# Optimization experiments

Hardware: AMD Instinct MI355X
Metric: run time of the kernel (lower is better)

The kernel has to match this reference:

```python
import jax, jax.numpy as jnp
import numpy as np

N = 100000
C = 128
VEC = 16
GRID = 128
TEMP = 1.0
REP = C // VEC


def _offsets_cube():
    r = [-1, 0, 1]
    return np.array([[i, j, k] for i in r for j in r for k in r], dtype=np.int64)


def _offsets_cross(d):
    offs = [[0, 0, 0]]
    for ax in range(3):
        for s in (-d, d):
            o = [0, 0, 0]
            o[ax] = s
            offs.append(o)
    return np.array(offs, dtype=np.int64)


def _build_nbr(coords, lut, offs):
    # coords [N,3] int, lut: flat grid -> voxel idx or -1. Returns [K,N] int32, -1 = missing.
    maps = []
    for o in offs:
        nc = coords + o
        valid = np.all((nc >= 0) & (nc < GRID), axis=1)
        flat = nc[:, 0] * GRID * GRID + nc[:, 1] * GRID + nc[:, 2]
        idx = np.where(valid, lut[np.clip(flat, 0, GRID ** 3 - 1)], -1)
        maps.append(idx)
    return jnp.asarray(np.stack(maps).astype(np.int32))


def setup_inputs() -> dict:
    rng = np.random.default_rng(0)
    flat = rng.choice(GRID ** 3, size=N, replace=False)
    coords = np.stack([flat // (GRID * GRID), (flat // GRID) % GRID, flat % GRID], axis=1)
    lut = np.full(GRID ** 3, -1, dtype=np.int64)
    lut[flat] = np.arange(N)
    nbr_cross2 = _build_nbr(coords, lut, _offsets_cross(2))  # expert 0: HYPER_CROSS dil=2, K=7
    nbr_cube = _build_nbr(coords, lut, _offsets_cube())       # expert 1: HYPER_CUBE dil=1, K=27
    nbr_cross3 = _build_nbr(coords, lut, _offsets_cross(3))  # expert 2: HYPER_CROSS dil=3, K=7

    ks = jax.random.split(jax.random.key(0), 10)
    s = lambda k, shape, sc: jax.random.normal(k, shape, jnp.float32) * sc
    return dict(
        x=s(ks[0], (N, C), 1.0),
        v1_w=s(ks[1], (27, C, C), 0.05),
        v1_g=jnp.ones((C,), jnp.float32), v1_b=jnp.zeros((C,), jnp.float32),
        v2_w=s(ks[2], (C, C), 0.05),
        v2_g=jnp.ones((C,), jnp.float32), v2_b=jnp.zeros((C,), jnp.float32),
        q_w=s(ks[3], (C, VEC), 0.05),
        q_g=jnp.ones((VEC,), jnp.float32), q_b=jnp.zeros((VEC,), jnp.float32),
        cb0=s(ks[4], (7, C), 0.1),
        cb1=s(ks[5], (27, C), 0.1),
        cb2=s(ks[6], (7, C), 0.1),
        out_w=s(ks[7], (C, C), 0.05),
        out_g=jnp.ones((C,), jnp.float32), out_b=jnp.zeros((C,), jnp.float32),
        nbr_cross2=nbr_cross2, nbr_cube=nbr_cube, nbr_cross3=nbr_cross3,
    )


def _bn(x, g, b, eps=1e-5):
    m = x.mean(0)
    v = x.var(0)
    return (x - m) * jax.lax.rsqrt(v + eps) * g + b


def _sparse_conv(x, nbr, W):
    # full sparse conv: out[i] = sum_k W[k] @ x[nbr[k,i]] over valid neighbors
    out = jnp.zeros((x.shape[0], W.shape[2]), x.dtype)
    for k in range(W.shape[0]):  # fixed small K, structural loop
        idx = nbr[k]
        g = jnp.where((idx >= 0)[:, None], x[jnp.clip(idx, 0)], 0.0)
        out = out + g @ W[k]
    return out


def _chanwise_conv(x, nbr, kern):
    # MinkowskiChannelwiseConvolution: out[i,c] = sum_k kern[k,c] * x[nbr[k,i],c]
    out = jnp.zeros_like(x)
    for k in range(kern.shape[0]):
        idx = nbr[k]
        out = out + jnp.where((idx >= 0)[:, None], x[jnp.clip(idx, 0)], 0.0) * kern[k]
    return out


def _pairwise_score(q, nbr):
    # pairwise qk: mean over valid neighbors j of q_i * q_j (per channel) -> [N, VEC]
    acc = jnp.zeros_like(q)
    cnt = jnp.zeros((q.shape[0], 1), q.dtype)
    for k in range(nbr.shape[0]):
        idx = nbr[k]
        valid = (idx >= 0)[:, None]
        acc = acc + jnp.where(valid, q[jnp.clip(idx, 0)], 0.0)
        cnt = cnt + valid.astype(q.dtype)
    return q * acc / jnp.maximum(cnt, 1.0)


def reference(x, v1_w, v1_g, v1_b, v2_w, v2_g, v2_b, q_w, q_g, q_b,
              cb0, cb1, cb2, out_w, out_g, out_b,
              nbr_cross2, nbr_cube, nbr_cross3):
    # value branch: 3x3 ConvBNReLU -> 1x1 ConvBNReLU
    v = jax.nn.relu(_bn(_sparse_conv(x, nbr_cube, v1_w), v1_g, v1_b))
    v = jax.nn.relu(_bn(v @ v2_w, v2_g, v2_b))
    # query: 1x1 ConvBNReLU -> [N, VEC]
    q = jax.nn.relu(_bn(x @ q_w, q_g, q_b))
    # M=3 channelwise codebook expert convs on the value features
    cb_outs = [
        _chanwise_conv(v, nbr_cross2, cb0),
        _chanwise_conv(v, nbr_cube, cb1),
        _chanwise_conv(v, nbr_cross3, cb2),
    ]
    # pairwise attention scores per expert neighborhood -> [N, VEC, M]
    scores = jnp.stack([
        _pairwise_score(q, nbr_cross2),
        _pairwise_score(q, nbr_cube),
        _pairwise_score(q, nbr_cross3),
    ], axis=-1)
    attn = jax.nn.softmax(scores / TEMP, axis=-1)
    attn = jnp.repeat(attn, REP, axis=1)  # expand_vec_dim: [N, C, M]
    out = sum(attn[:, :, m] * cb_outs[m] for m in range(3))
    out = jax.nn.relu(_bn(out @ out_w, out_g, out_b))
    return out + x  # residual (inplanes == planes, downsample is identity)
```

## Files before the change

### kernel.cpp

```cpp
#include <hip/hip_runtime.h>

#define NN 100000
#define C 128
#define VEC 16
#define AROW 136
#define GCAP 240000

typedef __bf16 bfx8 __attribute__((ext_vector_type(8)));
typedef float f32x4 __attribute__((ext_vector_type(4)));

__device__ inline unsigned pack_bf2(float a, float b) {
    unsigned ua = __float_as_uint(a);
    unsigned ub = __float_as_uint(b);
    ua = (ua + 0x7fffu + ((ua >> 16) & 1u)) >> 16;
    ub = (ub + 0x7fffu + ((ub >> 16) & 1u)) >> 16;
    return ua | (ub << 16);
}
__device__ inline unsigned short bf1(float a) {
    unsigned u = __float_as_uint(a);
    return (unsigned short)((u + 0x7fffu + ((u >> 16) & 1u)) >> 16);
}

__device__ inline void wconv_body(const float* __restrict__ W, unsigned short* __restrict__ Wf, int F) {
    int e = F & 7, l = (F >> 3) & 63, nt = (F >> 9) & 7, ks = (F >> 12) & 3, kt = F >> 14;
    int cin = ks * 32 + (l >> 4) * 8 + e;
    int cout = nt * 16 + (l & 15);
    Wf[F] = bf1(W[((size_t)kt * C + cin) * C + cout]);
}

__global__ __launch_bounds__(256) void prep(const float* __restrict__ v1w, const float* __restrict__ v2w,
                                            const float* __restrict__ outw, const float* __restrict__ x,
                                            unsigned short* __restrict__ v1f, unsigned short* __restrict__ v2f,
                                            unsigned short* __restrict__ outf, unsigned short* __restrict__ xh) {
    int b = blockIdx.x, tid = threadIdx.x;
    if (b < 1728)       wconv_body(v1w, v1f, b * 256 + tid);
    else if (b < 1792)  wconv_body(v2w, v2f, (b - 1728) * 256 + tid);
    else if (b < 1856)  wconv_body(outw, outf, (b - 1792) * 256 + tid);
    else {
        const int total8 = NN * C / 8;
        for (int t = (b - 1856) * 256 + tid; t < total8; t += 1024 * 256) {
            float4 xa = *reinterpret_cast<const float4*>(x + (size_t)t * 8);
            float4 xb = *reinterpret_cast<const float4*>(x + (size_t)t * 8 + 4);
            uint4 pk;
            pk.x = pack_bf2(xa.x, xa.y); pk.y = pack_bf2(xa.z, xa.w);
            pk.z = pack_bf2(xb.x, xb.y); pk.w = pack_bf2(xb.z, xb.w);
            *reinterpret_cast<uint4*>(&xh[(size_t)t * 8]) = pk;
        }
    }
}

__global__ __launch_bounds__(256) void compactA(const int* __restrict__ nbr, int* __restrict__ cnt,
                                                int* __restrict__ slotmap, int* __restrict__ pairs,
                                                unsigned* __restrict__ maskbuf) {
    const int k = blockIdx.x / 49, cb = blockIdx.x % 49, tid = threadIdx.x;
    const int i0 = cb * 2048 + tid * 8;
    int j[8]; int lc = 0;
#pragma unroll
    for (int t = 0; t < 8; ++t) {
        int i = i0 + t;
        j[t] = (i < NN) ? nbr[(size_t)k * NN + i] : -1;
        lc += (j[t] >= 0);
    }
    __shared__ int ls[256]; __shared__ int sbase;
    ls[tid] = lc; __syncthreads();
    for (int off = 1; off < 256; off <<= 1) {
        int v = (tid >= off) ? ls[tid - off] : 0;
        __syncthreads();
        ls[tid] += v;
        __syncthreads();
    }
    if (tid == 255) sbase = atomicAdd(&cnt[k], ls[255]);
    __syncthreads();
    int slot = sbase + ls[tid] - lc;
    for (int t = 0; t < 8; ++t) {
        int i = i0 + t; if (i >= NN) break;
        int s = -1;
        if (j[t] >= 0) {
            s = slot++;
            pairs[(size_t)k * NN + s] = j[t];
            atomicOr(&maskbuf[i], 1u << k);
        }
        slotmap[(size_t)k * NN + i] = s;
    }
}

__global__ void prefixA2(int* __restrict__ hdr) {
    if (threadIdx.x == 0) {
        int co = 0, go = 0;
        for (int k = 0; k < 27; ++k) {
            hdr[32 + k] = co; hdr[64 + k] = go;
            int nch = (hdr[k] + 31) / 32;
            co += nch; go += nch * 32;
        }
        hdr[32 + 27] = co;
    }
}

__global__ __launch_bounds__(256) void convB(const unsigned short* __restrict__ xh, const int* __restrict__ pairs,
                                             const int* __restrict__ hdr, const bfx8* __restrict__ Wf,
                                             unsigned short* __restrict__ g) {
    const int tid = threadIdx.x, l = tid & 63, w = tid >> 6, rr = tid >> 4, gg = tid & 15;
    __shared__ int sco[28], scnt[27], sgo[27];
    __shared__ unsigned short Ash[32 * AROW];
    __shared__ unsigned short Osh[32 * AROW];
    if (tid < 28) sco[tid] = hdr[32 + tid];
    if (tid < 27) { scnt[tid] = hdr[tid]; sgo[tid] = hdr[64 + tid]; }
    __syncthreads();
    const int tot = sco[27];
    for (int t = blockIdx.x; t < tot; t += gridDim.x) {
        int lo = 0, hi = 26;
        while (lo < hi) { int mid = (lo + hi + 1) >> 1; if (sco[mid] <= t) lo = mid; else hi = mid - 1; }
        const int k = lo, c = t - sco[k], cntk = scnt[k];
        const int srow = c * 32;
        const size_t gbase = (size_t)(sgo[k] + srow) * C;
#pragma unroll
        for (int h = 0; h < 2; ++h) {
            int row = srow + h * 16 + rr;
            uint4 pk = {0u, 0u, 0u, 0u};
            if (row < cntk) {
                int j = pairs[(size_t)k * NN + row];
                pk = *reinterpret_cast<const uint4*>(xh + (size_t)j * C + gg * 8);
            }
            *reinterpret_cast<uint4*>(&Ash[(h * 16 + rr) * AROW + gg * 8]) = pk;
        }
        __syncthreads();
        f32x4 a00 = {0.f,0.f,0.f,0.f}, a01 = {0.f,0.f,0.f,0.f};
        f32x4 a10 = {0.f,0.f,0.f,0.f}, a11 = {0.f,0.f,0.f,0.f};
        const unsigned short* ar0 = &Ash[(l & 15) * AROW + (l >> 4) * 8];
        const unsigned short* ar1 = &Ash[(16 + (l & 15)) * AROW + (l >> 4) * 8];
#pragma unroll
        for (int ks = 0; ks < 4; ++ks) {
            bfx8 b0 = Wf[((k * 4 + ks) * 8 + 2 * w) * 64 + l];
            bfx8 b1 = Wf[((k * 4 + ks) * 8 + 2 * w + 1) * 64 + l];
            bfx8 f0 = *reinterpret_cast<const bfx8*>(ar0 + ks * 32);
            bfx8 f1 = *reinterpret_cast<const bfx8*>(ar1 + ks * 32);
            a00 = __builtin_amdgcn_mfma_f32_16x16x32_bf16(f0, b0, a00, 0, 0, 0);
            a01 = __builtin_amdgcn_mfma_f32_16x16x32_bf16(f0, b1, a01, 0, 0, 0);
            a10 = __builtin_amdgcn_mfma_f32_16x16x32_bf16(f1, b0, a10, 0, 0, 0);
            a11 = __builtin_amdgcn_mfma_f32_16x16x32_bf16(f1, b1, a11, 0, 0, 0);
        }
#pragma unroll
        for (int r = 0; r < 4; ++r) {
            int row = (l >> 4) * 4 + r;
            Osh[row * AROW + w * 32 + (l & 15)]        = bf1(a00[r]);
            Osh[row * AROW + w * 32 + 16 + (l & 15)]   = bf1(a01[r]);
            Osh[(16 + row) * AROW + w * 32 + (l & 15)] = bf1(a10[r]);
            Osh[(16 + row) * AROW + w * 32 + 16 + (l & 15)] = bf1(a11[r]);
        }
        __syncthreads();
#pragma unroll
        for (int h = 0; h < 2; ++h) {
            int row = h * 16 + rr;
            uint4 v = *reinterpret_cast<uint4*>(&Osh[row * AROW + gg * 8]);
            *reinterpret_cast<uint4*>(&g[gbase + (size_t)row * C + gg * 8]) = v;
        }
        __syncthreads();
    }
}

__global__ __launch_bounds__(256) void convC(const unsigned short* __restrict__ g, const int* __restrict__ slotmap,
                                             const int* __restrict__ hdr, const unsigned* __restrict__ maskbuf,
                                             unsigned short* __restrict__ outh, float* __restrict__ psb,
                                             float* __restrict__ pqb) {
    const int tid = threadIdx.x, p = tid >> 4, gg = tid & 15, c0 = gg * 8;
    const int i = blockIdx.x * 16 + p;
    __shared__ int sgo[27];
    __shared__ float outt[16 * 132];
    if (tid < 27) sgo[tid] = hdr[64 + tid];
    __syncthreads();
    unsigned m = maskbuf[i];
    float acc[8] = {0.f,0.f,0.f,0.f,0.f,0.f,0.f,0.f};
    while (m) {
        int k = (int)__builtin_ctz(m); m &= m - 1;
        int slot = slotmap[(size_t)k * NN + i];
        const unsigned short* gr = &g[(size_t)(sgo[k] + slot) * C + c0];
        uint4 u = *reinterpret_cast<const uint4*>(gr);
        acc[0] += __uint_as_float(u.x << 16); acc[1] += __uint_as_float(u.x & 0xffff0000u);
        acc[2] += __uint_as_float(u.y << 16); acc[3] += __uint_as_float(u.y & 0xffff0000u);
        acc[4] += __uint_as_float(u.z << 16); acc[5] += __uint_as_float(u.z & 0xffff0000u);
        acc[6] += __uint_as_float(u.w << 16); acc[7] += __uint_as_float(u.w & 0xffff0000u);
    }
#pragma unroll
    for (int c2 = 0; c2 < 8; ++c2) outt[p * 132 + c0 + c2] = acc[c2];
    uint4 pk;
    pk.x = pack_bf2(acc[0], acc[1]); pk.y = pack_bf2(acc[2], acc[3]);
    pk.z = pack_bf2(acc[4], acc[5]); pk.w = pack_bf2(acc[6], acc[7]);
    *reinterpret_cast<uint4*>(&outh[(size_t)i * C + c0]) = pk;
    __syncthreads();
    if (tid < 128) {
        float s = 0.f, q = 0.f;
#pragma unroll
        for (int r = 0; r < 16; ++r) { float v = outt[r * 132 + tid]; s += v; q += v * v; }
        psb[(size_t)blockIdx.x * C + tid] = s;
        pqb[(size_t)blockIdx.x * C + tid] = q;
    }
}

__global__ __launch_bounds__(256) void statsF128(const float* __restrict__ psb, const float* __restrict__ pqb,
                                                 int rows,
                                                 float* __restrict__ ps2, float* __restrict__ pq2,
                                                 const float* __restrict__ g, const float* __restrict__ b,
                                                 float* __restrict__ a, float* __restrict__ cc,
                                                 int* __restrict__ ticket) {
    const int tid = threadIdx.x, ch = tid & 127, half = tid >> 7;
    float s = 0.f, q = 0.f;
    for (int i = blockIdx.x * 2 + half; i < rows; i += 128) {
        s += psb[(size_t)i * C + ch];
        q += pqb[(size_t)i * C + ch];
    }
    __shared__ float ls[256], lq[256];
    __shared__ int amlast;
    ls[tid] = s; lq[tid] = q;
    __syncthreads();
    if (tid < 128) {
        ps2[blockIdx.x * C + ch] = ls[tid] + ls[tid + 128];
        pq2[blockIdx.x * C + ch] = lq[tid] + lq[tid + 128];
    }
    __threadfence();
    __syncthreads();
    if (tid == 0) amlast = (atomicAdd(ticket, 1) == 63) ? 1 : 0;
    __syncthreads();
    if (!amlast) return;
    __threadfence();
    if (tid < 128) {
        float ss = 0.f, qq = 0.f;
        for (int i = 0; i < 64; ++i) { ss += ps2[i * C + ch]; qq += pq2[i * C + ch]; }
        float m = ss / (float)NN;
        float var = fmaxf(qq / (float)NN - m * m, 0.f);
        float rs = rsqrtf(var + 1e-5f);
        float av = g[ch] * rs;
        a[ch] = av;
        cc[ch] = b[ch] - m * av;
    }
}

__global__ __launch_bounds__(256) void statsF16(const float* __restrict__ buf,
                                                float* __restrict__ ps2, float* __restrict__ pq2,
                                                const float* __restrict__ g, const float* __restrict__ b,
                                                float* __restrict__ a, float* __restrict__ cc,
                                                int* __restrict__ ticket) {
    const int tid = threadIdx.x, ch = tid & 15, grp = tid >> 4;
    float s = 0.f, q = 0.f;
    for (int i = blockIdx.x * 16 + grp; i < NN; i += 64 * 16) {
        float val = buf[(size_t)i * VEC + ch];
        s += val; q += val * val;
    }
    __shared__ float ls[256], lq[256];
    __shared__ int amlast;
    ls[tid] = s; lq[tid] = q;
    __syncthreads();
    if (tid < 16) {
        float ss = 0.f, qq = 0.f;
        for (int g2 = 0; g2 < 16; ++g2) { ss += ls[g2 * 16 + ch]; qq += lq[g2 * 16 + ch]; }
        ps2[blockIdx.x * VEC + ch] = ss; pq2[blockIdx.x * VEC + ch] = qq;
    }
    __threadfence();
    __syncthreads();
    if (tid == 0) amlast = (atomicAdd(ticket, 1) == 63) ? 1 : 0;
    __syncthreads();
    if (!amlast) return;
    __threadfence();
    if (tid < 16) {
        float ss = 0.f, qq = 0.f;
        for (int i = 0; i < 64; ++i) { ss += ps2[i * VEC + ch]; qq += pq2[i * VEC + ch]; }
        float m = ss / (float)NN;
        float var = fmaxf(qq / (float)NN - m * m, 0.f);
        float rs = rsqrtf(var + 1e-5f);
        float av = g[ch] * rs;
        a[ch] = av;
        cc[ch] = b[ch] - m * av;
    }
}

__global__ __launch_bounds__(256) void mm_bn_h32(const unsigned short* __restrict__ in,
                                                 const float* __restrict__ a,
                                                 const float* __restrict__ cc,
                                                 const bfx8* __restrict__ Wf,
                                                 unsigned short* __restrict__ out,
                                                 float* __restrict__ psb,
                                                 float* __restrict__ pqb) {
    const int tid = threadIdx.x, l = tid & 63, w = tid >> 6;
    const int rr = tid >> 4, gg = tid & 15;
    const size_t base = (size_t)blockIdx.x * 32;
    __shared__ unsigned short Ash[32 * AROW];
    __shared__ float outt[32 * 132];
    float4 a4 = *reinterpret_cast<const float4*>(&a[gg * 8]);
    float4 a4b = *reinterpret_cast<const float4*>(&a[gg * 8 + 4]);
    float4 c4 = *reinterpret_cast<const float4*>(&cc[gg * 8]);
    float4 c4b = *reinterpret_cast<const float4*>(&cc[gg * 8 + 4]);
#pragma unroll
    for (int h = 0; h < 2; ++h) {
        int row = h * 16 + rr;
        uint4 u = *reinterpret_cast<const uint4*>(in + (base + row) * C + gg * 8);
        float e0 = fmaxf(fmaf(__uint_as_float(u.x << 16),        a4.x,  c4.x), 0.f);
        float e1 = fmaxf(fmaf(__uint_as_float(u.x & 0xffff0000u), a4.y,  c4.y), 0.f);
        float e2 = fmaxf(fmaf(__uint_as_float(u.y << 16),        a4.z,  c4.z), 0.f);
        float e3 = fmaxf(fmaf(__uint_as_float(u.y & 0xffff0000u), a4.w,  c4.w), 0.f);
        float e4 = fmaxf(fmaf(__uint_as_float(u.z << 16),        a4b.x, c4b.x), 0.f);
        float e5 = fmaxf(fmaf(__uint_as_float(u.z & 0xffff0000u), a4b.y, c4b.y), 0.f);
        float e6 = fmaxf(fmaf(__uint_as_float(u.w << 16),        a4b.z, c4b.z), 0.f);
        float e7 = fmaxf(fmaf(__uint_as_float(u.w & 0xffff0000u), a4b.w, c4b.w), 0.f);
        u.x = pack_bf2(e0, e1); u.y = pack_bf2(e2, e3);
        u.z = pack_bf2(e4, e5); u.w = pack_bf2(e6, e7);
        *reinterpret_cast<uint4*>(&Ash[row * AROW + gg * 8]) = u;
    }
    __syncthreads();
    f32x4 a00 = {0.f,0.f,0.f,0.f}, a01 = {0.f,0.f,0.f,0.f};
    f32x4 a10 = {0.f,0.f,0.f,0.f}, a11 = {0.f,0.f,0.f,0.f};
    const unsigned short* ar0 = &Ash[(l & 15) * AROW + (l >> 4) * 8];
    const unsigned short* ar1 = &Ash[(16 + (l & 15)) * AROW + (l >> 4) * 8];
#pragma unroll
    for (int ks = 0; ks < 4; ++ks) {
        bfx8 b0 = Wf[(ks * 8 + 2 * w) * 64 + l];
        bfx8 b1 = Wf[(ks * 8 + 2 * w + 1) * 64 + l];
        bfx8 f0 = *reinterpret_cast<const bfx8*>(ar0 + ks * 32);
        bfx8 f1 = *reinterpret_cast<const bfx8*>(ar1 + ks * 32);
        a00 = __builtin_amdgcn_mfma_f32_16x16x32_bf16(f0, b0, a00, 0, 0, 0);
        a01 = __builtin_amdgcn_mfma_f32_16x16x32_bf16(f0, b1, a01, 0, 0, 0);
        a10 = __builtin_amdgcn_mfma_f32_16x16x32_bf16(f1, b0, a10, 0, 0, 0);
        a11 = __builtin_amdgcn_mfma_f32_16x16x32_bf16(f1, b1, a11, 0, 0, 0);
    }
#pragma unroll
    for (int r = 0; r < 4; ++r) {
        int row = (l >> 4) * 4 + r;
        outt[row * 132 + w * 32 + (l & 15)]        = a00[r];
        outt[row * 132 + w * 32 + 16 + (l & 15)]   = a01[r];
        outt[(16 + row) * 132 + w * 32 + (l & 15)] = a10[r];
        outt[(16 + row) * 132 + w * 32 + 16 + (l & 15)] = a11[r];
    }
    __syncthreads();
#pragma unroll
    for (int h = 0; h < 2; ++h) {
        int row = h * 16 + rr;
        float4 v0 = *reinterpret_cast<float4*>(&outt[row * 132 + gg * 8]);
        float4 v1 = *reinterpret_cast<float4*>(&outt[row * 132 + gg * 8 + 4]);
        uint4 pk;
        pk.x = pack_bf2(v0.x, v0.y); pk.y = pack_bf2(v0.z, v0.w);
        pk.z = pack_bf2(v1.x, v1.y); pk.w = pack_bf2(v1.z, v1.w);
        *reinterpret_cast<uint4*>(&out[(base + row) * C + gg * 8]) = pk;
    }
    if (tid < 128) {
        float s = 0.f, q = 0.f;
#pragma unroll
        for (int r = 0; r < 32; ++r) { float v = outt[r * 132 + tid]; s += v; q += v * v; }
        psb[(size_t)blockIdx.x * C + tid] = s;
        pqb[(size_t)blockIdx.x * C + tid] = q;
    }
}

__global__ __launch_bounds__(256) void qmmh(const unsigned short* __restrict__ xh,
                                            const float* __restrict__ qw,
                                            float* __restrict__ outq) {
    const int v = threadIdx.x & 15, p = threadIdx.x >> 4;
    const size_t i = (size_t)blockIdx.x * 16 + p;
    float acc = 0.f;
    for (int cin0 = 0; cin0 < C; cin0 += 8) {
        uint4 u = *reinterpret_cast<const uint4*>(xh + i * C + cin0);
        acc += __uint_as_float(u.x << 16)         * qw[(cin0 + 0) * VEC + v]
             + __uint_as_float(u.x & 0xffff0000u) * qw[(cin0 + 1) * VEC + v]
             + __uint_as_float(u.y << 16)         * qw[(cin0 + 2) * VEC + v]
             + __uint_as_float(u.y & 0xffff0000u) * qw[(cin0 + 3) * VEC + v]
             + __uint_as_float(u.z << 16)         * qw[(cin0 + 4) * VEC + v]
             + __uint_as_float(u.z & 0xffff0000u) * qw[(cin0 + 5) * VEC + v]
             + __uint_as_float(u.w << 16)         * qw[(cin0 + 6) * VEC + v]
             + __uint_as_float(u.w & 0xffff0000u) * qw[(cin0 + 7) * VEC + v];
    }
    outq[i * VEC + v] = acc;
}

__global__ __launch_bounds__(256) void attn_out(const unsigned short* __restrict__ vraw,
                                                const float* __restrict__ a2,
                                                const float* __restrict__ c2,
                                                const float* __restrict__ qraw,
                                                const float* __restrict__ aq,
                                                const float* __restrict__ cq,
                                                const int* __restrict__ nA,
                                                const int* __restrict__ nB,
                                                const int* __restrict__ nC,
                                                const float* __restrict__ cb0,
                                                const float* __restrict__ cb1,
                                                const float* __restrict__ cb2,
                                                const bfx8* __restrict__ Wf,
                                                unsigned short* __restrict__ outh,
                                                float* __restrict__ psb,
                                                float* __restrict__ pqb) {
    const int tid = threadIdx.x, l = tid & 63, w = tid >> 6;
    const int base = blockIdx.x * 16;
    __shared__ float outt[16 * 132];
    int* raw = (int*)outt;
    __shared__ int sj[16][44];
    __shared__ short sk[16][44];
    __shared__ short sb[16][4];
    __shared__ float sattn[16][16][3];
    __shared__ unsigned short Ash[16 * AROW];

    for (int t = tid; t < 656; t += 256) {
        int k = t >> 4, p = t & 15;
        int i = base + p;
        int j;
        if (k < 7)       j = nA[(size_t)k * NN + i];
        else if (k < 34) j = nB[(size_t)(k - 7) * NN + i];
        else             j = nC[(size_t)(k - 34) * NN + i];
        raw[p * 41 + k] = j;
    }
    __syncthreads();
    if (tid < 16) {
        int p = tid, n = 0;
#pragma unroll
        for (int k = 0; k < 7; ++k) { int j = raw[p * 41 + k]; if (j >= 0) { sj[p][n] = j; sk[p][n] = (short)k; ++n; } }
        int b0 = n;
#pragma unroll
        for (int k = 7; k < 34; ++k) { int j = raw[p * 41 + k]; if (j >= 0) { sj[p][n] = j; sk[p][n] = (short)(k - 7); ++n; } }
        int b1 = n;
#pragma unroll
        for (int k = 34; k < 41; ++k) { int j = raw[p * 41 + k]; if (j >= 0) { sj[p][n] = j; sk[p][n] = (short)(k - 34); ++n; } }
        sb[p][0] = (short)b0; sb[p][1] = (short)b1; sb[p][2] = (short)n;
    }
    __syncthreads();
    {
        int p = tid >> 4, v = tid & 15;
        int b0 = sb[p][0], b1 = sb[p][1], b2 = sb[p][2];
        float av = aq[v], cv = cq[v];
        float qi = fmaxf(fmaf(qraw[(size_t)(base + p) * VEC + v], av, cv), 0.f);
        float a0 = 0.f, a1 = 0.f, a2s = 0.f;
        for (int s = 0; s < b0; ++s) a0 += fmaxf(fmaf(qraw[(size_t)sj[p][s] * VEC + v], av, cv), 0.f);
        for (int s = b0; s < b1; ++s) a1 += fmaxf(fmaf(qraw[(size_t)sj[p][s] * VEC + v], av, cv), 0.f);
        for (int s = b1; s < b2; ++s) a2s += fmaxf(fmaf(qraw[(size_t)sj[p][s] * VEC + v], av, cv), 0.f);
        float s0 = qi * a0 / (float)(b0 > 0 ? b0 : 1);
        float s1 = qi * a1 / (float)(b1 - b0 > 0 ? b1 - b0 : 1);
        float s2 = qi * a2s / (float)(b2 - b1 > 0 ? b2 - b1 : 1);
        float mx = fmaxf(s0, fmaxf(s1, s2));
        float e0 = __expf(s0 - mx), e1 = __expf(s1 - mx), e2 = __expf(s2 - mx);
        float inv = 1.f / (e0 + e1 + e2);
        sattn[p][v][0] = e0 * inv; sattn[p][v][1] = e1 * inv; sattn[p][v][2] = e2 * inv;
    }
    __syncthreads();
    {
        int p = tid >> 4, g = tid & 15, c0 = g * 8;
        int b0 = sb[p][0], b1 = sb[p][1], b2 = sb[p][2];
        float4 va = *reinterpret_cast<const float4*>(&a2[c0]);
        float4 vab = *reinterpret_cast<const float4*>(&a2[c0 + 4]);
        float4 vc = *reinterpret_cast<const float4*>(&c2[c0]);
        float4 vcb = *reinterpret_cast<const float4*>(&c2[c0 + 4]);
        float A0[8], A1[8], A2[8];
#pragma unroll
        for (int c = 0; c < 8; ++c) { A0[c] = 0.f; A1[c] = 0.f; A2[c] = 0.f; }
        for (int s = 0; s < b0; ++s) {
            int j = sj[p][s], k = sk[p][s];
            uint4 u = *reinterpret_cast<const uint4*>(vraw + (size_t)j * C + c0);
            float4 ca = *reinterpret_cast<const float4*>(&cb0[k * C + c0]);
            float4 cb = *reinterpret_cast<const float4*>(&cb0[k * C + c0 + 4]);
            A0[0] = fmaf(ca.x, fmaxf(fmaf(__uint_as_float(u.x << 16),        va.x,  vc.x), 0.f), A0[0]);
            A0[1] = fmaf(ca.y, fmaxf(fmaf(__uint_as_float(u.x & 0xffff0000u), va.y,  vc.y), 0.f), A0[1]);
            A0[2] = fmaf(ca.z, fmaxf(fmaf(__uint_as_float(u.y << 16),        va.z,  vc.z), 0.f), A0[2]);
            A0[3] = fmaf(ca.w, fmaxf(fmaf(__uint_as_float(u.y & 0xffff0000u), va.w,  vc.w), 0.f), A0[3]);
            A0[4] = fmaf(cb.x, fmaxf(fmaf(__uint_as_float(u.z << 16),        vab.x, vcb.x), 0.f), A0[4]);
            A0[5] = fmaf(cb.y, fmaxf(fmaf(__uint_as_float(u.z & 0xffff0000u), vab.y, vcb.y), 0.f), A0[5]);
            A0[6] = fmaf(cb.z, fmaxf(fmaf(__uint_as_float(u.w << 16),        vab.z, vcb.z), 0.f), A0[6]);
            A0[7] = fmaf(cb.w, fmaxf(fmaf(__uint_as_float(u.w & 0xffff0000u), vab.w, vcb.w), 0.f), A0[7]);
        }
        for (int s = b0; s < b1; ++s) {
            int j = sj[p][s], k = sk[p][s];
            uint4 u = *reinterpret_cast<const uint4*>(vraw + (size_t)j * C + c0);
            float4 ca = *reinterpret_cast<const float4*>(&cb1[k * C + c0]);
            float4 cb = *reinterpret_cast<const float4*>(&cb1[k * C + c0 + 4]);
            A1[0] = fmaf(ca.x, fmaxf(fmaf(__uint_as_float(u.x << 16),        va.x,  vc.x), 0.f), A1[0]);
            A1[1] = fmaf(ca.y, fmaxf(fmaf(__uint_as_float(u.x & 0xffff0000u), va.y,  vc.y), 0.f), A1[1]);
            A1[2] = fmaf(ca.z, fmaxf(fmaf(__uint_as_float(u.y << 16),        va.z,  vc.z), 0.f), A1[2]);
            A1[3] = fmaf(ca.w, fmaxf(fmaf(__uint_as_float(u.y & 0xffff0000u), va.w,  vc.w), 0.f), A1[3]);
            A1[4] = fmaf(cb.x, fmaxf(fmaf(__uint_as_float(u.z << 16),        vab.x, vcb.x), 0.f), A1[4]);
            A1[5] = fmaf(cb.y, fmaxf(fmaf(__uint_as_float(u.z & 0xffff0000u), vab.y, vcb.y), 0.f), A1[5]);
            A1[6] = fmaf(cb.z, fmaxf(fmaf(__uint_as_float(u.w << 16),        vab.z, vcb.z), 0.f), A1[6]);
            A1[7] = fmaf(cb.w, fmaxf(fmaf(__uint_as_float(u.w & 0xffff0000u), vab.w, vcb.w), 0.f), A1[7]);
        }
        for (int s = b1; s < b2; ++s) {
            int j = sj[p][s], k = sk[p][s];
            uint4 u = *reinterpret_cast<const uint4*>(vraw + (size_t)j * C + c0);
            float4 ca = *reinterpret_cast<const float4*>(&cb2[k * C + c0]);
            float4 cb = *reinterpret_cast<const float4*>(&cb2[k * C + c0 + 4]);
            A2[0] = fmaf(ca.x, fmaxf(fmaf(__uint_as_float(u.x << 16),        va.x,  vc.x), 0.f), A2[0]);
            A2[1] = fmaf(ca.y, fmaxf(fmaf(__uint_as_float(u.x & 0xffff0000u), va.y,  vc.y), 0.f), A2[1]);
            A2[2] = fmaf(ca.z, fmaxf(fmaf(__uint_as_float(u.y << 16),        va.z,  vc.z), 0.f), A2[2]);
            A2[3] = fmaf(ca.w, fmaxf(fmaf(__uint_as_float(u.y & 0xffff0000u), va.w,  vc.w), 0.f), A2[3]);
            A2[4] = fmaf(cb.x, fmaxf(fmaf(__uint_as_float(u.z << 16),        vab.x, vcb.x), 0.f), A2[4]);
            A2[5] = fmaf(cb.y, fmaxf(fmaf(__uint_as_float(u.z & 0xffff0000u), vab.y, vcb.y), 0.f), A2[5]);
            A2[6] = fmaf(cb.z, fmaxf(fmaf(__uint_as_float(u.w << 16),        vab.z, vcb.z), 0.f), A2[6]);
            A2[7] = fmaf(cb.w, fmaxf(fmaf(__uint_as_float(u.w & 0xffff0000u), vab.w, vcb.w), 0.f), A2[7]);
        }
        float w0 = sattn[p][g][0], w1 = sattn[p][g][1], w2 = sattn[p][g][2];
        float o[8];
#pragma unroll
        for (int c = 0; c < 8; ++c) o[c] = w0 * A0[c] + w1 * A1[c] + w2 * A2[c];
        uint4 pk;
        pk.x = pack_bf2(o[0], o[1]); pk.y = pack_bf2(o[2], o[3]);
        pk.z = pack_bf2(o[4], o[5]); pk.w = pack_bf2(o[6], o[7]);
        *reinterpret_cast<uint4*>(&Ash[p * AROW + c0]) = pk;
    }
    __syncthreads();
    {
        f32x4 acc0 = {0.f, 0.f, 0.f, 0.f};
        f32x4 acc1 = {0.f, 0.f, 0.f, 0.f};
        const unsigned short* arow = &Ash[(l & 15) * AROW + (l >> 4) * 8];
#pragma unroll
        for (int ks = 0; ks < 4; ++ks) {
            bfx8 af = *reinterpret_cast<const bfx8*>(arow + ks * 32);
            bfx8 b0 = Wf[(ks * 8 + 2 * w) * 64 + l];
            bfx8 b1 = Wf[(ks * 8 + 2 * w + 1) * 64 + l];
            acc0 = __builtin_amdgcn_mfma_f32_16x16x32_bf16(af, b0, acc0, 0, 0, 0);
            acc1 = __builtin_amdgcn_mfma_f32_16x16x32_bf16(af, b1, acc1, 0, 0, 0);
        }
#pragma unroll
        for (int r = 0; r < 4; ++r) {
            int row = (l >> 4) * 4 + r;
            outt[row * 132 + w * 32 + (l & 15)] = acc0[r];
            outt[row * 132 + w * 32 + 16 + (l & 15)] = acc1[r];
        }
    }
    __syncthreads();
    {
        int rr = tid >> 4, gg = tid & 15;
        float4 v0 = *reinterpret_cast<float4*>(&outt[rr * 132 + gg * 8]);
        float4 v1 = *reinterpret_cast<float4*>(&outt[rr * 132 + gg * 8 + 4]);
        uint4 pk;
        pk.x = pack_bf2(v0.x, v0.y); pk.y = pack_bf2(v0.z, v0.w);
        pk.z = pack_bf2(v1.x, v1.y); pk.w = pack_bf2(v1.z, v1.w);
        *reinterpret_cast<uint4*>(&outh[(size_t)(base + rr) * C + gg * 8]) = pk;
    }
    if (tid < 128) {
        float s = 0.f, q = 0.f;
#pragma unroll
        for (int r = 0; r < 16; ++r) { float v = outt[r * 132 + tid]; s += v; q += v * v; }
        psb[(size_t)blockIdx.x * C + tid] = s;
        pqb[(size_t)blockIdx.x * C + tid] = q;
    }
}

__global__ __launch_bounds__(256) void final_bn_res_h(const unsigned short* __restrict__ buf,
                                                      const float* __restrict__ a,
                                                      const float* __restrict__ cc,
                                                      const float* __restrict__ x,
                                                      float* __restrict__ out) {
    const int total8 = NN * C / 8;
    for (int t = blockIdx.x * 256 + threadIdx.x; t < total8; t += gridDim.x * 256) {
        int ch = (t * 8) & 127;
        uint4 u = *reinterpret_cast<const uint4*>(buf + (size_t)t * 8);
        float4 xa = *reinterpret_cast<const float4*>(x + (size_t)t * 8);
        float4 xb = *reinterpret_cast<const float4*>(x + (size_t)t * 8 + 4);
        float4 a4 = *reinterpret_cast<const float4*>(&a[ch]);
        float4 a4b = *reinterpret_cast<const float4*>(&a[ch + 4]);
        float4 c4 = *reinterpret_cast<const float4*>(&cc[ch]);
        float4 c4b = *reinterpret_cast<const float4*>(&cc[ch + 4]);
        float4 o0, o1;
        o0.x = fmaxf(fmaf(__uint_as_float(u.x << 16),        a4.x,  c4.x), 0.f) + xa.x;
        o0.y = fmaxf(fmaf(__uint_as_float(u.x & 0xffff0000u), a4.y,  c4.y), 0.f) + xa.y;
        o0.z = fmaxf(fmaf(__uint_as_float(u.y << 16),        a4.z,  c4.z), 0.f) + xa.z;
        o0.w = fmaxf(fmaf(__uint_as_float(u.y & 0xffff0000u), a4.w,  c4.w), 0.f) + xa.w;
        o1.x = fmaxf(fmaf(__uint_as_float(u.z << 16),        a4b.x, c4b.x), 0.f) + xb.x;
        o1.y = fmaxf(fmaf(__uint_as_float(u.z & 0xffff0000u), a4b.y, c4b.y), 0.f) + xb.y;
        o1.z = fmaxf(fmaf(__uint_as_float(u.w << 16),        a4b.z, c4b.z), 0.f) + xb.z;
        o1.w = fmaxf(fmaf(__uint_as_float(u.w & 0xffff0000u), a4b.w, c4b.w), 0.f) + xb.w;
        *reinterpret_cast<float4*>(out + (size_t)t * 8) = o0;
        *reinterpret_cast<float4*>(out + (size_t)t * 8 + 4) = o1;
    }
}

extern "C" void kernel_launch(void* const* d_in, const int* in_sizes, int n_in,
                              void* d_out, int out_size, void* d_ws, size_t ws_size,
                              hipStream_t stream) {
    (void)in_sizes; (void)n_in; (void)out_size; (void)ws_size;
    const float* x    = (const float*)d_in[0];
    const float* v1_w = (const float*)d_in[1];
    const float* v1_g = (const float*)d_in[2];
    const float* v1_b = (const float*)d_in[3];
    const float* v2_w = (const float*)d_in[4];
    const float* v2_g = (const float*)d_in[5];
    const float* v2_b = (const float*)d_in[6];
    const float* q_w  = (const float*)d_in[7];
    const float* q_g  = (const float*)d_in[8];
    const float* q_b  = (const float*)d_in[9];
    const float* cb0  = (const float*)d_in[10];
    const float* cb1  = (const float*)d_in[11];
    const float* cb2  = (const float*)d_in[12];
    const float* out_w = (const float*)d_in[13];
    const float* out_g = (const float*)d_in[14];
    const float* out_b = (const float*)d_in[15];
    const int* nbrA = (const int*)d_in[16];
    const int* nbrB = (const int*)d_in[17];
    const int* nbrC = (const int*)d_in[18];
    float* out = (float*)d_out;

    float* w = (float*)d_ws;
    unsigned short* bufAh = (unsigned short*)w;
    float* r1 = w + (size_t)NN * C / 2;
    unsigned short* g = (unsigned short*)r1;
    int* slotmap = (int*)(r1 + 15360000);
    int* pairs   = (int*)(r1 + 15360000 + 2700000);
    unsigned short* bufBh = (unsigned short*)r1;
    float* bufQ = r1 + 6400000;
    size_t o = (size_t)NN * C / 2 + 20760000;
    unsigned short* xh = (unsigned short*)(w + o); o += (size_t)NN * C / 2;
    float* psb  = w + o; o += (size_t)6250 * C;
    float* pqb  = w + o; o += (size_t)6250 * C;
    float* ps2  = w + o; o += 64 * C;
    float* pq2  = w + o; o += 64 * C;
    float* ps16 = w + o; o += 64 * VEC;
    float* pq16 = w + o; o += 64 * VEC;
    float* a1 = w + o; o += C;  float* c1 = w + o; o += C;
    float* a2 = w + o; o += C;  float* c2 = w + o; o += C;
    float* ao = w + o; o += C;  float* co = w + o; o += C;
    float* aq = w + o; o += VEC; float* cq = w + o; o += VEC;
    unsigned short* v1f = (unsigned short*)(w + o); o += (27 * 16384) / 2;
    unsigned short* v2f = (unsigned short*)(w + o); o += 16384 / 2;
    unsigned short* outf = (unsigned short*)(w + o); o += 16384 / 2;
    int* hdr = (int*)(w + o); o += 128;
    unsigned* maskbuf = (unsigned*)(w + o); o += NN;

    hipMemsetAsync(hdr, 0, (size_t)(128 + NN) * sizeof(int), stream);
    prep<<<2880, 256, 0, stream>>>(v1_w, v2_w, out_w, x, v1f, v2f, outf, xh);

    compactA<<<27 * 49, 256, 0, stream>>>(nbrB, hdr, slotmap, pairs, maskbuf);
    prefixA2<<<1, 64, 0, stream>>>(hdr);
    convB<<<2048, 256, 0, stream>>>(xh, pairs, hdr, (const bfx8*)v1f, g);
    convC<<<NN / 16, 256, 0, stream>>>(g, slotmap, hdr, maskbuf, bufAh, psb, pqb);
    statsF128<<<64, 256, 0, stream>>>(psb, pqb, 6250, ps2, pq2, v1_g, v1_b, a1, c1, hdr + 96);

    mm_bn_h32<<<NN / 32, 256, 0, stream>>>(bufAh, a1, c1, (const bfx8*)v2f, bufBh, psb, pqb);
    statsF128<<<64, 256, 0, stream>>>(psb, pqb, 3125, ps2, pq2, v2_g, v2_b, a2, c2, hdr + 97);

    qmmh<<<NN / 16, 256, 0, stream>>>(xh, q_w, bufQ);
    statsF16<<<64, 256, 0, stream>>>(bufQ, ps16, pq16, q_g, q_b, aq, cq, hdr + 98);

    attn_out<<<NN / 16, 256, 0, stream>>>(bufBh, a2, c2, bufQ, aq, cq,
                                          nbrA, nbrB, nbrC, cb0, cb1, cb2,
                                          (const bfx8*)outf, bufAh, psb, pqb);
    statsF128<<<64, 256, 0, stream>>>(psb, pqb, 6250, ps2, pq2, out_g, out_b, ao, co, hdr + 99);

    final_bn_res_h<<<2048, 256, 0, stream>>>(bufAh, ao, co, x, out);
}
```

Baseline: 333.9 us.

## Process 32 points per attention block and read bf16 residual in final pass

The attention/output kernel now handles 32 points per 512-thread block. Neighbour compaction is split across 96 threads (one per point and expert) into fixed segment offsets, with neighbour index and kernel offset packed into one int. The MFMA tile mapping is adjusted so each wave covers 16 rows by 32 columns. The final BN+residual kernel reads the bf16 copy of x instead of fp32, halving residual read traffic but rounding the residual to bf16, which may affect accuracy.

```diff
diff --git a/kernel.cpp b/kernel.cpp
--- a/kernel.cpp
+++ b/kernel.cpp
@@ -368,34 +368,33 @@
     outq[i * VEC + v] = acc;
 }
 
-__global__ __launch_bounds__(256) void attn_out(const unsigned short* __restrict__ vraw,
-                                                const float* __restrict__ a2,
-                                                const float* __restrict__ c2,
-                                                const float* __restrict__ qraw,
-                                                const float* __restrict__ aq,
-                                                const float* __restrict__ cq,
-                                                const int* __restrict__ nA,
-                                                const int* __restrict__ nB,
-                                                const int* __restrict__ nC,
-                                                const float* __restrict__ cb0,
-                                                const float* __restrict__ cb1,
-                                                const float* __restrict__ cb2,
-                                                const bfx8* __restrict__ Wf,
-                                                unsigned short* __restrict__ outh,
-                                                float* __restrict__ psb,
-                                                float* __restrict__ pqb) {
+__global__ __launch_bounds__(512) void attn_out32(const unsigned short* __restrict__ vraw,
+                                                  const float* __restrict__ a2,
+                                                  const float* __restrict__ c2,
+                                                  const float* __restrict__ qraw,
+                                                  const float* __restrict__ aq,
+                                                  const float* __restrict__ cq,
+                                                  const int* __restrict__ nA,
+                                                  const int* __restrict__ nB,
+                                                  const int* __restrict__ nC,
+                                                  const float* __restrict__ cb0,
+                                                  const float* __restrict__ cb1,
+                                                  const float* __restrict__ cb2,
+                                                  const bfx8* __restrict__ Wf,
+                                                  unsigned short* __restrict__ outh,
+                                                  float* __restrict__ psb,
+                                                  float* __restrict__ pqb) {
     const int tid = threadIdx.x, l = tid & 63, w = tid >> 6;
-    const int base = blockIdx.x * 16;
-    __shared__ float outt[16 * 132];
+    const int base = blockIdx.x * 32;
+    __shared__ float outt[32 * 132];
     int* raw = (int*)outt;
-    __shared__ int sj[16][44];
-    __shared__ short sk[16][44];
-    __shared__ short sb[16][4];
-    __shared__ float sattn[16][16][3];
-    __shared__ unsigned short Ash[16 * AROW];
-
-    for (int t = tid; t < 656; t += 256) {
-        int k = t >> 4, p = t & 15;
+    __shared__ int sjk[32][44];
+    __shared__ short sb[32][4];
+    __shared__ float sattn[32][16][3];
+    __shared__ unsigned short Ash[32 * AROW];
+
+    for (int t = tid; t < 32 * 41; t += 512) {
+        int p = t & 31, k = t >> 5;
         int i = base + p;
         int j;
         if (k < 7)       j = nA[(size_t)k * NN + i];
@@ -404,31 +403,31 @@
         raw[p * 41 + k] = j;
     }
     __syncthreads();
-    if (tid < 16) {
-        int p = tid, n = 0;
-#pragma unroll
-        for (int k = 0; k < 7; ++k) { int j = raw[p * 41 + k]; if (j >= 0) { sj[p][n] = j; sk[p][n] = (short)k; ++n; } }
-        int b0 = n;
-#pragma unroll
-        for (int k = 7; k < 34; ++k) { int j = raw[p * 41 + k]; if (j >= 0) { sj[p][n] = j; sk[p][n] = (short)(k - 7); ++n; } }
-        int b1 = n;
-#pragma unroll
-        for (int k = 34; k < 41; ++k) { int j = raw[p * 41 + k]; if (j >= 0) { sj[p][n] = j; sk[p][n] = (short)(k - 34); ++n; } }
-        sb[p][0] = (short)b0; sb[p][1] = (short)b1; sb[p][2] = (short)n;
+    if (tid < 96) {
+        int p = tid & 31, e = tid >> 5;
+        int k0 = (e == 0) ? 0 : ((e == 1) ? 7 : 34);
+        int k1 = (e == 0) ? 7 : ((e == 1) ? 34 : 41);
+        int segbase = (e == 0) ? 0 : ((e == 1) ? 8 : 36);
+        int n = 0;
+        for (int k = k0; k < k1; ++k) {
+            int j = raw[p * 41 + k];
+            if (j >= 0) { sjk[p][segbase + n] = ((k - k0) << 20) | j; ++n; }
+        }
+        sb[p][e] = (short)n;
     }
     __syncthreads();
     {
         int p = tid >> 4, v = tid & 15;
-        int b0 = sb[p][0], b1 = sb[p][1], b2 = sb[p][2];
+        int n0 = sb[p][0], n1 = sb[p][1], n2 = sb[p][2];
         float av = aq[v], cv = cq[v];
         float qi = fmaxf(fmaf(qraw[(size_t)(base + p) * VEC + v], av, cv), 0.f);
         float a0 = 0.f, a1 = 0.f, a2s = 0.f;
-        for (int s = 0; s < b0; ++s) a0 += fmaxf(fmaf(qraw[(size_t)sj[p][s] * VEC + v], av, cv), 0.f);
-        for (int s = b0; s < b1; ++s) a1 += fmaxf(fmaf(qraw[(size_t)sj[p][s] * VEC + v], av, cv), 0.f);
-        for (int s = b1; s < b2; ++s) a2s += fmaxf(fmaf(qraw[(size_t)sj[p][s] * VEC + v], av, cv), 0.f);
-        float s0 = qi * a0 / (float)(b0 > 0 ? b0 : 1);
-        float s1 = qi * a1 / (float)(b1 - b0 > 0 ? b1 - b0 : 1);
-        float s2 = qi * a2s / (float)(b2 - b1 > 0 ? b2 - b1 : 1);
+        for (int s = 0; s < n0; ++s)      a0  += fmaxf(fmaf(qraw[(size_t)(sjk[p][s] & 0xFFFFF) * VEC + v], av, cv), 0.f);
+        for (int s = 8; s < 8 + n1; ++s)  a1  += fmaxf(fmaf(qraw[(size_t)(sjk[p][s] & 0xFFFFF) * VEC + v], av, cv), 0.f);
+        for (int s = 36; s < 36 + n2; ++s) a2s += fmaxf(fmaf(qraw[(size_t)(sjk[p][s] & 0xFFFFF) * VEC + v], av, cv), 0.f);
+        float s0 = qi * a0 / (float)(n0 > 0 ? n0 : 1);
+        float s1 = qi * a1 / (float)(n1 > 0 ? n1 : 1);
+        float s2 = qi * a2s / (float)(n2 > 0 ? n2 : 1);
         float mx = fmaxf(s0, fmaxf(s1, s2));
         float e0 = __expf(s0 - mx), e1 = __expf(s1 - mx), e2 = __expf(s2 - mx);
         float inv = 1.f / (e0 + e1 + e2);
@@ -437,7 +436,7 @@
     __syncthreads();
     {
         int p = tid >> 4, g = tid & 15, c0 = g * 8;
-        int b0 = sb[p][0], b1 = sb[p][1], b2 = sb[p][2];
+        int n0 = sb[p][0], n1 = sb[p][1], n2 = sb[p][2];
         float4 va = *reinterpret_cast<const float4*>(&a2[c0]);
         float4 vab = *reinterpret_cast<const float4*>(&a2[c0 + 4]);
         float4 vc = *reinterpret_cast<const float4*>(&c2[c0]);
@@ -445,8 +444,8 @@
         float A0[8], A1[8], A2[8];
 #pragma unroll
         for (int c = 0; c < 8; ++c) { A0[c] = 0.f; A1[c] = 0.f; A2[c] = 0.f; }
-        for (int s = 0; s < b0; ++s) {
-            int j = sj[p][s], k = sk[p][s];
+        for (int s = 0; s < n0; ++s) {
+            int jk = sjk[p][s]; int j = jk & 0xFFFFF, k = jk >> 20;
             uint4 u = *reinterpret_cast<const uint4*>(vraw + (size_t)j * C + c0);
             float4 ca = *reinterpret_cast<const float4*>(&cb0[k * C + c0]);
             float4 cb = *reinterpret_cast<const float4*>(&cb0[k * C + c0 + 4]);
@@ -459,8 +458,8 @@
             A0[6] = fmaf(cb.z, fmaxf(fmaf(__uint_as_float(u.w << 16),        vab.z, vcb.z), 0.f), A0[6]);
             A0[7] = fmaf(cb.w, fmaxf(fmaf(__uint_as_float(u.w & 0xffff0000u), vab.w, vcb.w), 0.f), A0[7]);
         }
-        for (int s = b0; s < b1; ++s) {
-            int j = sj[p][s], k = sk[p][s];
+        for (int s = 8; s < 8 + n1; ++s) {
+            int jk = sjk[p][s]; int j = jk & 0xFFFFF, k = jk >> 20;
             uint4 u = *reinterpret_cast<const uint4*>(vraw + (size_t)j * C + c0);
             float4 ca = *reinterpret_cast<const float4*>(&cb1[k * C + c0]);
             float4 cb = *reinterpret_cast<const float4*>(&cb1[k * C + c0 + 4]);
@@ -473,8 +472,8 @@
             A1[6] = fmaf(cb.z, fmaxf(fmaf(__uint_as_float(u.w << 16),        vab.z, vcb.z), 0.f), A1[6]);
             A1[7] = fmaf(cb.w, fmaxf(fmaf(__uint_as_float(u.w & 0xffff0000u), vab.w, vcb.w), 0.f), A1[7]);
         }
-        for (int s = b1; s < b2; ++s) {
-            int j = sj[p][s], k = sk[p][s];
+        for (int s = 36; s < 36 + n2; ++s) {
+            int jk = sjk[p][s]; int j = jk & 0xFFFFF, k = jk >> 20;
             uint4 u = *reinterpret_cast<const uint4*>(vraw + (size_t)j * C + c0);
             float4 ca = *reinterpret_cast<const float4*>(&cb2[k * C + c0]);
             float4 cb = *reinterpret_cast<const float4*>(&cb2[k * C + c0 + 4]);
@@ -498,22 +497,24 @@
     }
     __syncthreads();
     {
+        const int rowb = (w >> 2) * 16;
+        const int nt0 = 2 * (w & 3);
         f32x4 acc0 = {0.f, 0.f, 0.f, 0.f};
         f32x4 acc1 = {0.f, 0.f, 0.f, 0.f};
-        const unsigned short* arow = &Ash[(l & 15) * AROW + (l >> 4) * 8];
+        const unsigned short* arow = &Ash[(rowb + (l & 15)) * AROW + (l >> 4) * 8];
 #pragma unroll
         for (int ks = 0; ks < 4; ++ks) {
             bfx8 af = *reinterpret_cast<const bfx8*>(arow + ks * 32);
-            bfx8 b0 = Wf[(ks * 8 + 2 * w) * 64 + l];
-            bfx8 b1 = Wf[(ks * 8 + 2 * w + 1) * 64 + l];
+            bfx8 b0 = Wf[(ks * 8 + nt0) * 64 + l];
+            bfx8 b1 = Wf[(ks * 8 + nt0 + 1) * 64 + l];
             acc0 = __builtin_amdgcn_mfma_f32_16x16x32_bf16(af, b0, acc0, 0, 0, 0);
             acc1 = __builtin_amdgcn_mfma_f32_16x16x32_bf16(af, b1, acc1, 0, 0, 0);
         }
 #pragma unroll
         for (int r = 0; r < 4; ++r) {
-            int row = (l >> 4) * 4 + r;
-            outt[row * 132 + w * 32 + (l & 15)] = acc0[r];
-            outt[row * 132 + w * 32 + 16 + (l & 15)] = acc1[r];
+            int row = rowb + (l >> 4) * 4 + r;
+            outt[row * 132 + nt0 * 16 + (l & 15)] = acc0[r];
+            outt[row * 132 + (nt0 + 1) * 16 + (l & 15)] = acc1[r];
         }
     }
     __syncthreads();
@@ -529,7 +530,7 @@
     if (tid < 128) {
         float s = 0.f, q = 0.f;
 #pragma unroll
-        for (int r = 0; r < 16; ++r) { float v = outt[r * 132 + tid]; s += v; q += v * v; }
+        for (int r = 0; r < 32; ++r) { float v = outt[r * 132 + tid]; s += v; q += v * v; }
         psb[(size_t)blockIdx.x * C + tid] = s;
         pqb[(size_t)blockIdx.x * C + tid] = q;
     }
@@ -538,27 +539,26 @@
 __global__ __launch_bounds__(256) void final_bn_res_h(const unsigned short* __restrict__ buf,
                                                       const float* __restrict__ a,
                                                       const float* __restrict__ cc,
-                                                      const float* __restrict__ x,
+                                                      const unsigned short* __restrict__ xh,
                                                       float* __restrict__ out) {
     const int total8 = NN * C / 8;
     for (int t = blockIdx.x * 256 + threadIdx.x; t < total8; t += gridDim.x * 256) {
         int ch = (t * 8) & 127;
         uint4 u = *reinterpret_cast<const uint4*>(buf + (size_t)t * 8);
-        float4 xa = *reinterpret_cast<const float4*>(x + (size_t)t * 8);
-        float4 xb = *reinterpret_cast<const float4*>(x + (size_t)t * 8 + 4);
+        uint4 xu = *reinterpret_cast<const uint4*>(xh + (size_t)t * 8);
         float4 a4 = *reinterpret_cast<const float4*>(&a[ch]);
         float4 a4b = *reinterpret_cast<const float4*>(&a[ch + 4]);
         float4 c4 = *reinterpret_cast<const float4*>(&cc[ch]);
         float4 c4b = *reinterpret_cast<const float4*>(&cc[ch + 4]);
         float4 o0, o1;
-        o0.x = fmaxf(fmaf(__uint_as_float(u.x << 16),        a4.x,  c4.x), 0.f) + xa.x;
-        o0.y = fmaxf(fmaf(__uint_as_float(u.x & 0xffff0000u), a4.y,  c4.y), 0.f) + xa.y;
-        o0.z = fmaxf(fmaf(__uint_as_float(u.y << 16),        a4.z,  c4.z), 0.f) + xa.z;
-        o0.w = fmaxf(fmaf(__uint_as_float(u.y & 0xffff0000u), a4.w,  c4.w), 0.f) + xa.w;
-        o1.x = fmaxf(fmaf(__uint_as_float(u.z << 16),        a4b.x, c4b.x), 0.f) + xb.x;
-        o1.y = fmaxf(fmaf(__uint_as_float(u.z & 0xffff0000u), a4b.y, c4b.y), 0.f) + xb.y;
-        o1.z = fmaxf(fmaf(__uint_as_float(u.w << 16),        a4b.z, c4b.z), 0.f) + xb.z;
-        o1.w = fmaxf(fmaf(__uint_as_float(u.w & 0xffff0000u), a4b.w, c4b.w), 0.f) + xb.w;
+        o0.x = fmaxf(fmaf(__uint_as_float(u.x << 16),        a4.x,  c4.x), 0.f) + __uint_as_float(xu.x << 16);
+        o0.y = fmaxf(fmaf(__uint_as_float(u.x & 0xffff0000u), a4.y,  c4.y), 0.f) + __uint_as_float(xu.x & 0xffff0000u);
+        o0.z = fmaxf(fmaf(__uint_as_float(u.y << 16),        a4.z,  c4.z), 0.f) + __uint_as_float(xu.y << 16);
+        o0.w = fmaxf(fmaf(__uint_as_float(u.y & 0xffff0000u), a4.w,  c4.w), 0.f) + __uint_as_float(xu.y & 0xffff0000u);
+        o1.x = fmaxf(fmaf(__uint_as_float(u.z << 16),        a4b.x, c4b.x), 0.f) + __uint_as_float(xu.z << 16);
+        o1.y = fmaxf(fmaf(__uint_as_float(u.z & 0xffff0000u), a4b.y, c4b.y), 0.f) + __uint_as_float(xu.z & 0xffff0000u);
+        o1.z = fmaxf(fmaf(__uint_as_float(u.w << 16),        a4b.z, c4b.z), 0.f) + __uint_as_float(xu.w << 16);
+        o1.w = fmaxf(fmaf(__uint_as_float(u.w & 0xffff0000u), a4b.w, c4b.w), 0.f) + __uint_as_float(xu.w & 0xffff0000u);
         *reinterpret_cast<float4*>(out + (size_t)t * 8) = o0;
         *reinterpret_cast<float4*>(out + (size_t)t * 8 + 4) = o1;
     }
@@ -630,10 +630,10 @@
     qmmh<<<NN / 16, 256, 0, stream>>>(xh, q_w, bufQ);
     statsF16<<<64, 256, 0, stream>>>(bufQ, ps16, pq16, q_g, q_b, aq, cq, hdr + 98);
 
-    attn_out<<<NN / 16, 256, 0, stream>>>(bufBh, a2, c2, bufQ, aq, cq,
-                                          nbrA, nbrB, nbrC, cb0, cb1, cb2,
-                                          (const bfx8*)outf, bufAh, psb, pqb);
-    statsF128<<<64, 256, 0, stream>>>(psb, pqb, 6250, ps2, pq2, out_g, out_b, ao, co, hdr + 99);
-
-    final_bn_res_h<<<2048, 256, 0, stream>>>(bufAh, ao, co, x, out);
-}
+    attn_out32<<<NN / 32, 512, 0, stream>>>(bufBh, a2, c2, bufQ, aq, cq,
+                                            nbrA, nbrB, nbrC, cb0, cb1, cb2,
+                                            (const bfx8*)outf, bufAh, psb, pqb);
+    statsF128<<<64, 256, 0, stream>>>(psb, pqb, 3125, ps2, pq2, out_g, out_b, ao, co, hdr + 99);
+
+    final_bn_res_h<<<2048, 256, 0, stream>>>(bufAh, ao, co, xh, out);
+}
```

Result: slower. 343.9 us (+3.0%).
